# Kernel tuning notes

Hardware: AMD Instinct MI355X
Metric: run time of the kernel (lower is better)

The kernel has to match this reference:

```python
import jax, jax.numpy as jnp
import numpy as np

NZ, NX, NY = 128, 256, 256
N_GAUSS = 50000
SIGMA_CUTOFF = 3.0
R = 3  # hardcoded stencil radius in voxelize()


def setup_inputs() -> dict:
    key = jax.random.key(0)
    k1, k2, k3, k4 = jax.random.split(key, 4)
    centers = jax.random.uniform(k1, (N_GAUSS, 3), jnp.float32) * 2.0 - 1.0
    log_scales = jnp.full((N_GAUSS, 3), -4.0, jnp.float32)
    rho_real = jax.random.normal(k2, (N_GAUSS,), jnp.float32) * 0.1
    rho_imag = jax.random.normal(k3, (N_GAUSS,), jnp.float32) * 0.1
    # k-space undersampling mask (0/1)
    mask = (jax.random.uniform(k4, (NZ, NX, NY), jnp.float32) < 0.3).astype(jnp.float32)
    return {"mask": mask, "centers": centers, "log_scales": log_scales,
            "rho_real": rho_real, "rho_imag": rho_imag}


def _voxelize(centers, log_scales, rho_real, rho_imag):
    gr = jnp.arange(-R, R + 1)
    kz, kx, ky = jnp.meshgrid(gr, gr, gr, indexing='ij')
    offsets = jnp.stack([kz, kx, ky], axis=-1).reshape(-1, 3)  # [K,3], K=343
    dims = jnp.array([NZ, NX, NY], jnp.int32)
    gsm1 = (dims - 1).astype(jnp.float32)  # grid_size - 1
    # nearest voxel of each gaussian center ([-1,1] -> grid coords)
    ci = jnp.round((centers + 1.0) * 0.5 * gsm1).astype(jnp.int32)  # [M,3]
    ni = ci[:, None, :] + offsets[None, :, :]                        # [M,K,3]
    in_bounds = jnp.all((ni >= 0) & (ni < dims), axis=-1)            # [M,K]
    # neighbor coords back in normalized [-1,1] space
    nc = ni.astype(jnp.float32) / gsm1 * 2.0 - 1.0                   # [M,K,3]
    scales = jnp.exp(log_scales)
    delta = (nc - centers[:, None, :]) / (scales[:, None, :] + 1e-8)
    dist_sq = jnp.sum(delta * delta, axis=-1)                        # [M,K]
    valid = in_bounds & (dist_sq <= SIGMA_CUTOFF ** 2)
    w = jnp.where(valid, jnp.exp(-0.5 * dist_sq), 0.0)               # [M,K]
    vals_r = (rho_real[:, None] * w).ravel()
    vals_i = (rho_imag[:, None] * w).ravel()
    # clip indices for safety; invalid entries contribute 0
    nic = jnp.clip(ni, 0, dims - 1)
    flat = ((nic[..., 0] * NX + nic[..., 1]) * NY + nic[..., 2]).ravel()
    vol_r = jnp.zeros(NZ * NX * NY, jnp.float32).at[flat].add(vals_r).reshape(NZ, NX, NY)
    vol_i = jnp.zeros(NZ * NX * NY, jnp.float32).at[flat].add(vals_i).reshape(NZ, NX, NY)
    return vol_r + 1j * vol_i


def _image_to_kspace(vol):
    # centered orthonormal 3D FFT (standard MRI convention)
    return jnp.fft.fftshift(jnp.fft.fftn(jnp.fft.ifftshift(vol), norm='ortho'))


def reference(mask, centers, log_scales, rho_real, rho_imag):
    volume = _voxelize(centers, log_scales, rho_real, rho_imag)
    kspace_pred = mask * _image_to_kspace(volume)
    return (volume, kspace_pred)
```

## Files before the change

kernel.cpp:

```cpp
#include <hip/hip_runtime.h>
#include <math.h>

#define NZd 128
#define NXd 256
#define NYd 256
#define NVOX (NZd * NXd * NYd)
#define PI_F 3.14159265358979323846f
#define SCALE_ORTHO 3.4526698300124393e-4f
#define CAP 512

__global__ void zero_kernel(float4* __restrict__ p, int n4) {
    int i = blockIdx.x * blockDim.x + threadIdx.x;
    if (i < n4) p[i] = make_float4(0.f, 0.f, 0.f, 0.f);
}
__global__ void zero_ints_kernel(int* __restrict__ p, int n) {
    int i = blockIdx.x * blockDim.x + threadIdx.x;
    if (i < n) p[i] = 0;
}

__global__ void voxelize_kernel(const float* __restrict__ centers,
                                const float* __restrict__ log_scales,
                                const float* __restrict__ rho_r,
                                const float* __restrict__ rho_i,
                                float* __restrict__ vol, int M) {
    long long t = (long long)blockIdx.x * blockDim.x + threadIdx.x;
    if (t >= (long long)M * 343) return;
    int g = (int)(t / 343);
    int k = (int)(t % 343);
    int oz = k / 49 - 3, ox = (k / 7) % 7 - 3, oy = k % 7 - 3;
    float cz = centers[g * 3 + 0], cx = centers[g * 3 + 1], cy = centers[g * 3 + 2];
    int iz = (int)rintf((cz + 1.0f) * 0.5f * 127.0f);
    int ix = (int)rintf((cx + 1.0f) * 0.5f * 255.0f);
    int iy = (int)rintf((cy + 1.0f) * 0.5f * 255.0f);
    int nz = iz + oz, nx = ix + ox, ny = iy + oy;
    if (nz < 0 || nz >= NZd || nx < 0 || nx >= NXd || ny < 0 || ny >= NYd) return;
    float sz = expf(log_scales[g * 3 + 0]) + 1e-8f;
    float sx = expf(log_scales[g * 3 + 1]) + 1e-8f;
    float sy = expf(log_scales[g * 3 + 2]) + 1e-8f;
    float dz = ((float)nz / 127.0f * 2.0f - 1.0f - cz) / sz;
    float dx = ((float)nx / 255.0f * 2.0f - 1.0f - cx) / sx;
    float dy = ((float)ny / 255.0f * 2.0f - 1.0f - cy) / sy;
    float d2 = dz * dz + dx * dx + dy * dy;
    if (d2 > 9.0f) return;
    float w = expf(-0.5f * d2);
    int idx = (nz * NXd + nx) * NYd + ny;
    atomicAdd(&vol[2 * idx + 0], rho_r[g] * w);
    atomicAdd(&vol[2 * idx + 1], rho_i[g] * w);
}

__global__ void copy_real_kernel(const float2* __restrict__ cvol,
                                 float* __restrict__ out) {
    int i = blockIdx.x * blockDim.x + threadIdx.x;
    out[i] = cvol[i].x;
}

__device__ __forceinline__ void center_voxel(const float* __restrict__ centers,
                                             int g, int& iz, int& ix, int& iy) {
    float cz = centers[g * 3 + 0], cx = centers[g * 3 + 1], cy = centers[g * 3 + 2];
    iz = min(max((int)rintf((cz + 1.0f) * 0.5f * 127.0f), 0), 127);
    ix = min(max((int)rintf((cx + 1.0f) * 0.5f * 255.0f), 0), 255);
    iy = min(max((int)rintf((cy + 1.0f) * 0.5f * 255.0f), 0), 255);
}

__global__ void bin_count_kernel(const float* __restrict__ centers,
                                 int* __restrict__ cnt, int M) {
    int g = blockIdx.x * blockDim.x + threadIdx.x;
    if (g >= M) return;
    int iz, ix, iy;
    center_voxel(centers, g, iz, ix, iy);
    atomicAdd(&cnt[((iz >> 4) << 8) | ((ix >> 4) << 4) | (iy >> 4)], 1);
}

__global__ void bin_scan_kernel(const int* __restrict__ cnt,
                                int* __restrict__ off,
                                int* __restrict__ cursor) {
    int lane = threadIdx.x;
    int base = lane << 5;
    int s = 0;
    #pragma unroll
    for (int i = 0; i < 32; i++) s += cnt[base + i];
    int incl = s;
    #pragma unroll
    for (int d = 1; d < 64; d <<= 1) {
        int v = __shfl_up(incl, d, 64);
        if (lane >= d) incl += v;
    }
    int run = incl - s;
    for (int i = 0; i < 32; i++) {
        int c = cnt[base + i];
        off[base + i] = run;
        cursor[base + i] = run;
        run += c;
    }
}

__global__ void bin_scatter_kernel(const float* __restrict__ centers,
                                   const float* __restrict__ log_scales,
                                   const float* __restrict__ rho_r,
                                   const float* __restrict__ rho_i,
                                   int* __restrict__ cursor,
                                   int* __restrict__ ciA,
                                   float* __restrict__ czA, float* __restrict__ cxA,
                                   float* __restrict__ cyA,
                                   float* __restrict__ iszA, float* __restrict__ isxA,
                                   float* __restrict__ isyA,
                                   float* __restrict__ rrA, float* __restrict__ riA,
                                   int M) {
    int g = blockIdx.x * blockDim.x + threadIdx.x;
    if (g >= M) return;
    int iz, ix, iy;
    center_voxel(centers, g, iz, ix, iy);
    int b = ((iz >> 4) << 8) | ((ix >> 4) << 4) | (iy >> 4);
    int pos = atomicAdd(&cursor[b], 1);
    ciA[pos] = (iz << 16) | (ix << 8) | iy;
    czA[pos] = centers[g * 3 + 0];
    cxA[pos] = centers[g * 3 + 1];
    cyA[pos] = centers[g * 3 + 2];
    iszA[pos] = 1.0f / (expf(log_scales[g * 3 + 0]) + 1e-8f);
    isxA[pos] = 1.0f / (expf(log_scales[g * 3 + 1]) + 1e-8f);
    isyA[pos] = 1.0f / (expf(log_scales[g * 3 + 2]) + 1e-8f);
    rrA[pos] = rho_r[g];
    riA[pos] = rho_i[g];
}

__global__ __launch_bounds__(256) void tile_accum_kernel(
        const int* __restrict__ cnt, const int* __restrict__ off,
        const int* __restrict__ ciA,
        const float* __restrict__ czA, const float* __restrict__ cxA,
        const float* __restrict__ cyA,
        const float* __restrict__ iszA, const float* __restrict__ isxA,
        const float* __restrict__ isyA,
        const float* __restrict__ rrA, const float* __restrict__ riA,
        float2* __restrict__ cvol, float* __restrict__ out_vr) {
    __shared__ int   sci[CAP];
    __shared__ float scz[CAP], scx[CAP], scy[CAP];
    __shared__ float sisz[CAP], sisx[CAP], sisy[CAP];
    __shared__ float srr[CAP], sri[CAP];
    __shared__ int wcnt[4];

    int tile = blockIdx.x;
    int ty = tile & 15, tx = (tile >> 4) & 15, tz = tile >> 8;
    int z0 = tz << 4, x0 = tx << 4, y0 = ty << 4;
    int t = threadIdx.x;
    int lane = t & 63, wid = t >> 6;
    int yl = t & 15, xl = t >> 4;
    int nx = x0 + xl, ny = y0 + yl;
    float nxf = (float)nx * (2.0f / 255.0f) - 1.0f;
    float nyf = (float)ny * (2.0f / 255.0f) - 1.0f;

    float accR[16], accI[16];
    #pragma unroll
    for (int i = 0; i < 16; i++) { accR[i] = 0.f; accI[i] = 0.f; }

    int lc = 0;
    int byl = max(ty - 1, 0), byh = min(ty + 1, 15);

    for (int dzb = -1; dzb <= 1; dzb++) {
        int bz = tz + dzb;
        if ((unsigned)bz >= 8u) continue;
        for (int dxb = -1; dxb <= 1; dxb++) {
            int bx = tx + dxb;
            if ((unsigned)bx >= 16u) continue;
            int bl = (bz << 8) | (bx << 4) | byl;
            int bh = (bz << 8) | (bx << 4) | byh;
            int qs = off[bl];
            int qe = off[bh] + cnt[bh];
            for (int q0 = qs; q0 < qe; q0 += 256) {
                int q = q0 + t;
                bool keep = false;
                int cpv = 0;
                float czv, cxv, cyv, iszv, isxv, isyv, rrv, riv;
                if (q < qe) {
                    cpv = ciA[q];
                    int iz = cpv >> 16, ix = (cpv >> 8) & 255, iy = cpv & 255;
                    keep = !(ix + 3 < x0 || ix > x0 + 18 ||
                             iy + 3 < y0 || iy > y0 + 18 ||
                             iz + 3 < z0 || iz > z0 + 18);
                }
                if (keep) {
                    czv = czA[q]; cxv = cxA[q]; cyv = cyA[q];
                    iszv = iszA[q]; isxv = isxA[q]; isyv = isyA[q];
                    rrv = rrA[q]; riv = riA[q];
                }
                unsigned long long m = __ballot(keep);
                if (lane == 0) wcnt[wid] = __popcll(m);
                __syncthreads();
                int ntot = wcnt[0] + wcnt[1] + wcnt[2] + wcnt[3];
                int basew = lc;
                #pragma unroll
                for (int w = 0; w < 4; w++) if (w < wid) basew += wcnt[w];
                if (keep) {
                    int pos = basew + __popcll(m & ((1ULL << lane) - 1));
                    sci[pos] = cpv;
                    scz[pos] = czv; scx[pos] = cxv; scy[pos] = cyv;
                    sisz[pos] = iszv; sisx[pos] = isxv; sisy[pos] = isyv;
                    srr[pos] = rrv; sri[pos] = riv;
                }
                __syncthreads();
                lc += ntot;
                if (lc >= CAP - 256) {
                    for (int u = 0; u < lc; u++) {
                        int cp = sci[u];
                        int iz = cp >> 16, ix = (cp >> 8) & 255, iy = cp & 255;
                        int dxi = nx - ix, dyi = ny - iy;
                        if (dxi < -3 || dxi > 3 || dyi < -3 || dyi > 3) continue;
                        float dxv = (nxf - scx[u]) * sisx[u];
                        float dyv = (nyf - scy[u]) * sisy[u];
                        float dxy2 = dxv * dxv + dyv * dyv;
                        if (dxy2 > 9.0f) continue;
                        float cz_ = scz[u], isz_ = sisz[u];
                        float rr = srr[u], ri = sri[u];
                        int zlo = max(z0, iz - 3) - z0;
                        int zhi = min(z0 + 15, iz + 3) - z0;
                        #pragma unroll
                        for (int zl = 0; zl < 16; zl++) {
                            if (zl >= zlo && zl <= zhi) {
                                float zf = (float)(z0 + zl) * (2.0f / 127.0f) - 1.0f;
                                float dzv = (zf - cz_) * isz_;
                                float d2 = dxy2 + dzv * dzv;
                                if (d2 <= 9.0f) {
                                    float w = __expf(-0.5f * d2);
                                    accR[zl] += rr * w;
                                    accI[zl] += ri * w;
                                }
                            }
                        }
                    }
                    __syncthreads();
                    lc = 0;
                }
            }
        }
    }
    for (int u = 0; u < lc; u++) {
        int cp = sci[u];
        int iz = cp >> 16, ix = (cp >> 8) & 255, iy = cp & 255;
        int dxi = nx - ix, dyi = ny - iy;
        if (dxi < -3 || dxi > 3 || dyi < -3 || dyi > 3) continue;
        float dxv = (nxf - scx[u]) * sisx[u];
        float dyv = (nyf - scy[u]) * sisy[u];
        float dxy2 = dxv * dxv + dyv * dyv;
        if (dxy2 > 9.0f) continue;
        float cz_ = scz[u], isz_ = sisz[u];
        float rr = srr[u], ri = sri[u];
        int zlo = max(z0, iz - 3) - z0;
        int zhi = min(z0 + 15, iz + 3) - z0;
        #pragma unroll
        for (int zl = 0; zl < 16; zl++) {
            if (zl >= zlo && zl <= zhi) {
                float zf = (float)(z0 + zl) * (2.0f / 127.0f) - 1.0f;
                float dzv = (zf - cz_) * isz_;
                float d2 = dxy2 + dzv * dzv;
                if (d2 <= 9.0f) {
                    float w = __expf(-0.5f * d2);
                    accR[zl] += rr * w;
                    accI[zl] += ri * w;
                }
            }
        }
    }

    #pragma unroll
    for (int zl = 0; zl < 16; zl++) {
        size_t idx = ((size_t)(z0 + zl) * NXd + nx) * NYd + ny;
        cvol[idx] = make_float2(accR[zl], accI[zl]);
        out_vr[idx] = accR[zl];
    }
}

template <int L>
__device__ __forceinline__ void fft_lds(float2* buf) {
    int tid = threadIdx.x;
    for (int half = 1; half < L; half <<= 1) {
        __syncthreads();
        int j = tid & (half - 1);
        int i0 = ((tid ^ j) << 1) | j;
        int i1 = i0 + half;
        float ang = -PI_F * (float)j / (float)half;
        float s, c;
        sincosf(ang, &s, &c);
        float2 a = buf[i0];
        float2 b = buf[i1];
        float tr = c * b.x - s * b.y;
        float ti = c * b.y + s * b.x;
        buf[i0] = make_float2(a.x + tr, a.y + ti);
        buf[i1] = make_float2(a.x - tr, a.y - ti);
    }
    __syncthreads();
}

__global__ void fft_y_kernel(const float2* __restrict__ src,
                             float2* __restrict__ dst) {
    __shared__ float2 buf[256];
    __shared__ float2 tw[128];
    int l = blockIdx.x;
    int tid = threadIdx.x;
    {
        float s, c;
        sincosf(-PI_F * (float)tid / 128.0f, &s, &c);
        tw[tid] = make_float2(c, s);
    }
    int p = ((l >> 8) + l) & 1;
    const float2* s = src + (size_t)l * NYd;
    for (int i = tid; i < 256; i += 128) {
        float2 v = s[i];
        if ((p + i) & 1) { v.x = -v.x; v.y = -v.y; }
        buf[__brev((unsigned)i) >> 24] = v;
    }
    #pragma unroll
    for (int st = 0; st < 8; st++) {
        const int half = 1 << st;
        const int twstep = 128 >> st;
        __syncthreads();
        int j = tid & (half - 1);
        int i0 = ((tid ^ j) << 1) | j;
        int i1 = i0 + half;
        float2 w = tw[j * twstep];
        float2 a = buf[i0];
        float2 b = buf[i1];
        float tr = w.x * b.x - w.y * b.y;
        float ti = w.x * b.y + w.y * b.x;
        buf[i0] = make_float2(a.x + tr, a.y + ti);
        buf[i1] = make_float2(a.x - tr, a.y - ti);
    }
    __syncthreads();
    float2* d = dst + (size_t)l * NYd;
    for (int i = tid; i < 256; i += 128) d[i] = buf[i];
}

__global__ void fft_x_kernel(float2* __restrict__ ks) {
    __shared__ float2 buf[256];
    int l = blockIdx.x;
    int tid = threadIdx.x;
    int z = l >> 8, y = l & 255;
    float2* base = ks + (size_t)z * (NXd * NYd) + y;
    for (int i = tid; i < 256; i += 128)
        buf[__brev((unsigned)i) >> 24] = base[(size_t)i * NYd];
    fft_lds<256>(buf);
    for (int i = tid; i < 256; i += 128)
        base[(size_t)i * NYd] = buf[i];
}
__global__ void fft_z_kernel(float2* __restrict__ ks,
                             const float* __restrict__ mask,
                             float* __restrict__ out_real) {
    __shared__ float2 buf[128];
    int l = blockIdx.x;
    int tid = threadIdx.x;
    float2* base = ks + l;
    for (int i = tid; i < 128; i += 64)
        buf[__brev((unsigned)i) >> 25] = base[(size_t)i * (NXd * NYd)];
    fft_lds<128>(buf);
    int p = ((l >> 8) + l) & 1;
    for (int i = tid; i < 128; i += 64) {
        float2 v = buf[i];
        float sgn = ((p + i) & 1) ? -SCALE_ORTHO : SCALE_ORTHO;
        float m = mask[(size_t)i * (NXd * NYd) + l] * sgn;
        if (out_real) {
            out_real[(size_t)i * (NXd * NYd) + l] = v.x * m;
        } else {
            v.x *= m; v.y *= m;
            base[(size_t)i * (NXd * NYd)] = v;
        }
    }
}

__global__ __launch_bounds__(256) void fft_x8_kernel(float2* __restrict__ ks) {
    __shared__ float2 buf[8][256 + 1];
    __shared__ float2 tw[128];
    int t = threadIdx.x;
    int blk = blockIdx.x;
    int z = blk >> 5;
    int y8 = (blk & 31) << 3;
    if (t < 128) {
        float s, c;
        sincosf(-PI_F * (float)t / 128.0f, &s, &c);
        tw[t] = make_float2(c, s);
    }
    float2* base = ks + (size_t)z * (NXd * NYd) + y8;
    int yl = t & 7, xe0 = t >> 3;
    #pragma unroll
    for (int p = 0; p < 8; p++) {
        int xe = xe0 + (p << 5);
        float2 v = base[(size_t)xe * NYd + yl];
        buf[yl][__brev((unsigned)xe) >> 24] = v;
    }
    int s_ = t & 127;
    int fb0 = t >> 7;
    #pragma unroll
    for (int st = 0; st < 8; st++) {
        const int half = 1 << st;
        const int twstep = 128 >> st;
        __syncthreads();
        int j = s_ & (half - 1);
        int i0 = ((s_ ^ j) << 1) | j;
        int i1 = i0 + half;
        float2 w = tw[j * twstep];
        #pragma unroll
        for (int u = 0; u < 4; u++) {
            int fb = fb0 + (u << 1);
            float2 a = buf[fb][i0];
            float2 b = buf[fb][i1];
            float tr = w.x * b.x - w.y * b.y;
            float ti = w.x * b.y + w.y * b.x;
            buf[fb][i0] = make_float2(a.x + tr, a.y + ti);
            buf[fb][i1] = make_float2(a.x - tr, a.y - ti);
        }
    }
    __syncthreads();
    #pragma unroll
    for (int p = 0; p < 8; p++) {
        int xe = xe0 + (p << 5);
        base[(size_t)xe * NYd + yl] = buf[yl][xe];
    }
}

__global__ __launch_bounds__(256) void fft_z16_kernel(const float2* __restrict__ ks,
                                                      const float* __restrict__ mask,
                                                      float* __restrict__ out_kr) {
    __shared__ float2 buf[16][128 + 1];
    __shared__ float2 tw[64];
    int t = threadIdx.x;
    int blk = blockIdx.x;
    int kx = blk >> 4;
    int ky16 = (blk & 15) << 4;
    if (t < 64) {
        float s, c;
        sincosf(-PI_F * (float)t / 64.0f, &s, &c);
        tw[t] = make_float2(c, s);
    }
    const float2* base = ks + (size_t)kx * NYd + ky16;
    int kyl = t & 15, ze0 = t >> 4;
    #pragma unroll
    for (int p = 0; p < 8; p++) {
        int ze = ze0 + (p << 4);
        float2 v = base[(size_t)ze * (NXd * NYd) + kyl];
        buf[kyl][__brev((unsigned)ze) >> 25] = v;
    }
    int s_ = t & 63;
    int fb0 = t >> 6;
    #pragma unroll
    for (int st = 0; st < 7; st++) {
        const int half = 1 << st;
        const int twstep = 64 >> st;
        __syncthreads();
        int j = s_ & (half - 1);
        int i0 = ((s_ ^ j) << 1) | j;
        int i1 = i0 + half;
        float2 w = tw[j * twstep];
        #pragma unroll
        for (int u = 0; u < 4; u++) {
            int fb = fb0 + (u << 2);
            float2 a = buf[fb][i0];
            float2 b = buf[fb][i1];
            float tr = w.x * b.x - w.y * b.y;
            float ti = w.x * b.y + w.y * b.x;
            buf[fb][i0] = make_float2(a.x + tr, a.y + ti);
            buf[fb][i1] = make_float2(a.x - tr, a.y - ti);
        }
    }
    __syncthreads();
    int ky = ky16 + kyl;
    #pragma unroll
    for (int p = 0; p < 8; p++) {
        int ze = ze0 + (p << 4);
        float2 v = buf[kyl][ze];
        size_t gi = (size_t)ze * (NXd * NYd) + (size_t)kx * NYd + ky;
        float sgn = ((ze + kx + ky) & 1) ? -SCALE_ORTHO : SCALE_ORTHO;
        out_kr[gi] = v.x * (mask[gi] * sgn);
    }
}

extern "C" void kernel_launch(void* const* d_in, const int* in_sizes, int n_in,
                              void* d_out, int out_size, void* d_ws, size_t ws_size,
                              hipStream_t stream) {
    const float* mask       = (const float*)d_in[0];
    const float* centers    = (const float*)d_in[1];
    const float* log_scales = (const float*)d_in[2];
    const float* rho_r      = (const float*)d_in[3];
    const float* rho_i      = (const float*)d_in[4];
    int M = in_sizes[1] / 3;

    bool inter = (out_size >= 4 * NVOX);
    if (!inter) {
        if (out_size < 2 * NVOX || ws_size < (size_t)NVOX * 8) {
            int z4 = out_size / 4;
            if (z4 > 0)
                zero_kernel<<<(z4 + 255) / 256, 256, 0, stream>>>((float4*)d_out, z4);
            return;
        }
        float* out_vr = (float*)d_out;
        float* out_kr = out_vr + NVOX;
        float2* cvol = (float2*)d_ws;

        int Mpad = (M + 63) & ~63;
        bool fast = (8192 + 9LL * Mpad) <= (long long)NVOX;
        if (fast) {
            int* ibase  = (int*)out_kr;
            int* cnt    = ibase;
            int* off    = ibase + 2048;
            int* cursor = ibase + 4096;
            float* fbase = (float*)(ibase + 8192);
            int*   ciA  = (int*)fbase;
            float* czA  = fbase + 1LL * Mpad;
            float* cxA  = fbase + 2LL * Mpad;
            float* cyA  = fbase + 3LL * Mpad;
            float* iszA = fbase + 4LL * Mpad;
            float* isxA = fbase + 5LL * Mpad;
            float* isyA = fbase + 6LL * Mpad;
            float* rrA  = fbase + 7LL * Mpad;
            float* riA  = fbase + 8LL * Mpad;

            zero_ints_kernel<<<8, 256, 0, stream>>>(cnt, 2048);
            bin_count_kernel<<<(M + 255) / 256, 256, 0, stream>>>(centers, cnt, M);
            bin_scan_kernel<<<1, 64, 0, stream>>>(cnt, off, cursor);
            bin_scatter_kernel<<<(M + 255) / 256, 256, 0, stream>>>(
                centers, log_scales, rho_r, rho_i, cursor,
                ciA, czA, cxA, cyA, iszA, isxA, isyA, rrA, riA, M);
            tile_accum_kernel<<<2048, 256, 0, stream>>>(
                cnt, off, ciA, czA, cxA, cyA, iszA, isxA, isyA, rrA, riA,
                cvol, out_vr);
        } else {
            int n4 = (2 * NVOX) / 4;
            zero_kernel<<<(n4 + 255) / 256, 256, 0, stream>>>((float4*)cvol, n4);
            long long total = (long long)M * 343;
            int vb = (int)((total + 255) / 256);
            voxelize_kernel<<<vb, 256, 0, stream>>>(centers, log_scales, rho_r,
                                                    rho_i, (float*)cvol, M);
            copy_real_kernel<<<NVOX / 256, 256, 0, stream>>>(cvol, out_vr);
        }

        fft_y_kernel<<<NZd * NXd, 128, 0, stream>>>(cvol, cvol);
        fft_x8_kernel<<<NZd * 32, 256, 0, stream>>>(cvol);
        fft_z16_kernel<<<NXd * 16, 256, 0, stream>>>(cvol, mask, out_kr);
    } else {
        float2* cvol = (float2*)d_out;
        float2* cks  = cvol + NVOX;
        int n4 = (2 * NVOX) / 4;
        zero_kernel<<<(n4 + 255) / 256, 256, 0, stream>>>((float4*)cvol, n4);
        long long total = (long long)M * 343;
        int vb = (int)((total + 255) / 256);
        voxelize_kernel<<<vb, 256, 0, stream>>>(centers, log_scales, rho_r,
                                                rho_i, (float*)cvol, M);
        fft_y_kernel<<<NZd * NXd, 128, 0, stream>>>(cvol, cks);
        fft_x_kernel<<<NZd * NYd, 128, 0, stream>>>(cks);
        fft_z_kernel<<<NXd * NYd, 64, 0, stream>>>(cks, mask, nullptr);
    }
}
```

Before: 232.2 us.

## Scatter gaussian-voxel pairs into LDS accumulators instead of per-voxel gather

Changes the tile accumulation from a gather scheme, where each thread owns a 16-voxel z column and loops over every cached gaussian, to a scatter scheme. In the new scheme threads enumerate (gaussian, stencil offset) pairs and atomically add into a 16x16x16 LDS accumulator. This removes the per-thread serial scan over all candidate gaussians, most of which miss that thread's column. The cost is LDS atomics, integer div/mod per pair, 32KB of extra LDS (lower occupancy), and a smaller candidate cache (CAP 192) with an extra barrier per batch.

```diff
diff --git a/kernel.cpp b/kernel.cpp
--- a/kernel.cpp
+++ b/kernel.cpp
@@ -7,7 +7,7 @@
 #define NVOX (NZd * NXd * NYd)
 #define PI_F 3.14159265358979323846f
 #define SCALE_ORTHO 3.4526698300124393e-4f
-#define CAP 512
+#define CAP 192
 
 __global__ void zero_kernel(float4* __restrict__ p, int n4) {
     int i = blockIdx.x * blockDim.x + threadIdx.x;
@@ -123,6 +123,41 @@
     riA[pos] = rho_i[g];
 }
 
+__device__ __forceinline__ void process_pairs(
+        int lc, int z0, int x0, int y0, int t,
+        const int* sci, const float* scz, const float* scx, const float* scy,
+        const float* sisz, const float* sisx, const float* sisy,
+        const float* srr, const float* sri,
+        float* accR, float* accI) {
+    int total = lc * 343;
+    for (int p = t; p < total; p += 256) {
+        int u = p / 343;
+        int k = p - u * 343;
+        int cp = sci[u];
+        int iz = cp >> 16, ix = (cp >> 8) & 255, iy = cp & 255;
+        int oz = k / 49;
+        int r2 = k - oz * 49;
+        int ox = r2 / 7;
+        int oy = r2 - ox * 7;
+        int nz = iz + oz - 3, nx = ix + ox - 3, ny = iy + oy - 3;
+        int zl = nz - z0, xl = nx - x0, yl = ny - y0;
+        if ((unsigned)zl >= 16u || (unsigned)xl >= 16u || (unsigned)yl >= 16u)
+            continue;
+        float zf = (float)nz * (2.0f / 127.0f) - 1.0f;
+        float xf = (float)nx * (2.0f / 255.0f) - 1.0f;
+        float yf = (float)ny * (2.0f / 255.0f) - 1.0f;
+        float dzv = (zf - scz[u]) * sisz[u];
+        float dxv = (xf - scx[u]) * sisx[u];
+        float dyv = (yf - scy[u]) * sisy[u];
+        float d2 = dzv * dzv + dxv * dxv + dyv * dyv;
+        if (d2 > 9.0f) continue;
+        float w = __expf(-0.5f * d2);
+        int vi = (zl * 16 + xl) * 16 + yl;
+        atomicAdd(&accR[vi], srr[u] * w);
+        atomicAdd(&accI[vi], sri[u] * w);
+    }
+}
+
 __global__ __launch_bounds__(256) void tile_accum_kernel(
         const int* __restrict__ cnt, const int* __restrict__ off,
         const int* __restrict__ ciA,
@@ -132,6 +167,7 @@
         const float* __restrict__ isyA,
         const float* __restrict__ rrA, const float* __restrict__ riA,
         float2* __restrict__ cvol, float* __restrict__ out_vr) {
+    __shared__ float accR_lds[4096], accI_lds[4096];
     __shared__ int   sci[CAP];
     __shared__ float scz[CAP], scx[CAP], scy[CAP];
     __shared__ float sisz[CAP], sisx[CAP], sisy[CAP];
@@ -143,14 +179,8 @@
     int z0 = tz << 4, x0 = tx << 4, y0 = ty << 4;
     int t = threadIdx.x;
     int lane = t & 63, wid = t >> 6;
-    int yl = t & 15, xl = t >> 4;
-    int nx = x0 + xl, ny = y0 + yl;
-    float nxf = (float)nx * (2.0f / 255.0f) - 1.0f;
-    float nyf = (float)ny * (2.0f / 255.0f) - 1.0f;
-
-    float accR[16], accI[16];
-    #pragma unroll
-    for (int i = 0; i < 16; i++) { accR[i] = 0.f; accI[i] = 0.f; }
+
+    for (int v = t; v < 4096; v += 256) { accR_lds[v] = 0.f; accI_lds[v] = 0.f; }
 
     int lc = 0;
     int byl = max(ty - 1, 0), byh = min(ty + 1, 15);
@@ -165,12 +195,12 @@
             int bh = (bz << 8) | (bx << 4) | byh;
             int qs = off[bl];
             int qe = off[bh] + cnt[bh];
-            for (int q0 = qs; q0 < qe; q0 += 256) {
+            for (int q0 = qs; q0 < qe; q0 += CAP) {
                 int q = q0 + t;
                 bool keep = false;
                 int cpv = 0;
                 float czv, cxv, cyv, iszv, isxv, isyv, rrv, riv;
-                if (q < qe) {
+                if (t < CAP && q < qe) {
                     cpv = ciA[q];
                     int iz = cpv >> 16, ix = (cpv >> 8) & 255, iy = cpv & 255;
                     keep = !(ix + 3 < x0 || ix > x0 + 18 ||
@@ -183,9 +213,17 @@
                     rrv = rrA[q]; riv = riA[q];
                 }
                 unsigned long long m = __ballot(keep);
+                __syncthreads();
                 if (lane == 0) wcnt[wid] = __popcll(m);
                 __syncthreads();
                 int ntot = wcnt[0] + wcnt[1] + wcnt[2] + wcnt[3];
+                if (lc + ntot > CAP) {
+                    process_pairs(lc, z0, x0, y0, t, sci, scz, scx, scy,
+                                  sisz, sisx, sisy, srr, sri,
+                                  accR_lds, accI_lds);
+                    __syncthreads();
+                    lc = 0;
+                }
                 int basew = lc;
                 #pragma unroll
                 for (int w = 0; w < 4; w++) if (w < wid) basew += wcnt[w];
@@ -196,75 +234,21 @@
                     sisz[pos] = iszv; sisx[pos] = isxv; sisy[pos] = isyv;
                     srr[pos] = rrv; sri[pos] = riv;
                 }
-                __syncthreads();
                 lc += ntot;
-                if (lc >= CAP - 256) {
-                    for (int u = 0; u < lc; u++) {
-                        int cp = sci[u];
-                        int iz = cp >> 16, ix = (cp >> 8) & 255, iy = cp & 255;
-                        int dxi = nx - ix, dyi = ny - iy;
-                        if (dxi < -3 || dxi > 3 || dyi < -3 || dyi > 3) continue;
-                        float dxv = (nxf - scx[u]) * sisx[u];
-                        float dyv = (nyf - scy[u]) * sisy[u];
-                        float dxy2 = dxv * dxv + dyv * dyv;
-                        if (dxy2 > 9.0f) continue;
-                        float cz_ = scz[u], isz_ = sisz[u];
-                        float rr = srr[u], ri = sri[u];
-                        int zlo = max(z0, iz - 3) - z0;
-                        int zhi = min(z0 + 15, iz + 3) - z0;
-                        #pragma unroll
-                        for (int zl = 0; zl < 16; zl++) {
-                            if (zl >= zlo && zl <= zhi) {
-                                float zf = (float)(z0 + zl) * (2.0f / 127.0f) - 1.0f;
-                                float dzv = (zf - cz_) * isz_;
-                                float d2 = dxy2 + dzv * dzv;
-                                if (d2 <= 9.0f) {
-                                    float w = __expf(-0.5f * d2);
-                                    accR[zl] += rr * w;
-                                    accI[zl] += ri * w;
-                                }
-                            }
-                        }
-                    }
-                    __syncthreads();
-                    lc = 0;
-                }
             }
         }
     }
-    for (int u = 0; u < lc; u++) {
-        int cp = sci[u];
-        int iz = cp >> 16, ix = (cp >> 8) & 255, iy = cp & 255;
-        int dxi = nx - ix, dyi = ny - iy;
-        if (dxi < -3 || dxi > 3 || dyi < -3 || dyi > 3) continue;
-        float dxv = (nxf - scx[u]) * sisx[u];
-        float dyv = (nyf - scy[u]) * sisy[u];
-        float dxy2 = dxv * dxv + dyv * dyv;
-        if (dxy2 > 9.0f) continue;
-        float cz_ = scz[u], isz_ = sisz[u];
-        float rr = srr[u], ri = sri[u];
-        int zlo = max(z0, iz - 3) - z0;
-        int zhi = min(z0 + 15, iz + 3) - z0;
-        #pragma unroll
-        for (int zl = 0; zl < 16; zl++) {
-            if (zl >= zlo && zl <= zhi) {
-                float zf = (float)(z0 + zl) * (2.0f / 127.0f) - 1.0f;
-                float dzv = (zf - cz_) * isz_;
-                float d2 = dxy2 + dzv * dzv;
-                if (d2 <= 9.0f) {
-                    float w = __expf(-0.5f * d2);
-                    accR[zl] += rr * w;
-                    accI[zl] += ri * w;
-                }
-            }
-        }
-    }
-
-    #pragma unroll
-    for (int zl = 0; zl < 16; zl++) {
-        size_t idx = ((size_t)(z0 + zl) * NXd + nx) * NYd + ny;
-        cvol[idx] = make_float2(accR[zl], accI[zl]);
-        out_vr[idx] = accR[zl];
+    __syncthreads();
+    process_pairs(lc, z0, x0, y0, t, sci, scz, scx, scy,
+                  sisz, sisx, sisy, srr, sri, accR_lds, accI_lds);
+    __syncthreads();
+
+    for (int v = t; v < 4096; v += 256) {
+        int zl = v >> 8, xl = (v >> 4) & 15, yl = v & 15;
+        float r = accR_lds[v], im = accI_lds[v];
+        size_t idx = ((size_t)(z0 + zl) * NXd + (x0 + xl)) * NYd + (y0 + yl);
+        cvol[idx] = make_float2(r, im);
+        out_vr[idx] = r;
     }
 }
 
```

After: 353.0 us. 52.0% more time.
